# Kernel tuning notes

Measured on AMD Instinct MI355X. Metric: run time of the kernel, lower is better.

## Reference

```python
import jax, jax.numpy as jnp
import numpy as np

NUM_KNOTS = 10
DEGREE = 3
N_POINTS = 8_388_608


def make_knots():
    # Mirrors BSplineBasis.__init__: clamped knot vector on [0, 1]
    inner = np.linspace(0.0, 1.0, NUM_KNOTS - 2 * DEGREE)
    return np.concatenate([np.zeros(DEGREE), inner, np.ones(DEGREE)]).astype(np.float32)


def setup_inputs() -> dict:
    key = jax.random.key(0)
    x = jax.random.normal(key, (N_POINTS,), dtype=jnp.float32)
    knots = jnp.asarray(make_knots())  # [10]
    return {"x": x, "knots": knots}


def bspline_all_bases(x, t, degree):
    """Cox-de Boor recursion evaluating ALL basis functions in one fused pass.

    x: [N] points, t: [K] knots  ->  [N, K-degree-1] basis values.
    Matches scipy BSpline.basis_element per-knot evaluation (zero outside
    support; value 1 at the clamped right endpoint for the last basis).
    """
    K = t.shape[0]
    xe = x[:, None]                       # [N, 1]
    left, right = t[None, :-1], t[None, 1:]
    # degree-0: indicator of half-open interval [t_i, t_{i+1})
    B = ((xe >= left) & (xe < right)).astype(x.dtype)   # [N, K-1]
    # include global right endpoint in the last non-degenerate interval
    B = jnp.where((xe == t[-1]) & (right == t[-1]) & (left < right),
                  jnp.asarray(1.0, x.dtype), B)
    for d in range(1, degree + 1):        # fixed small loop (degree=3)
        tL, tLd = t[: K - d - 1], t[d : K - 1]    # t_i, t_{i+d}
        tR, tRd = t[1 : K - d], t[d + 1 : K]      # t_{i+1}, t_{i+d+1}
        den1 = tLd - tL
        den2 = tRd - tR
        safe1 = jnp.where(den1 > 0, den1, 1.0)
        safe2 = jnp.where(den2 > 0, den2, 1.0)
        w1 = jnp.where(den1[None] > 0, (xe - tL[None]) / safe1[None], 0.0)
        w2 = jnp.where(den2[None] > 0, (tRd[None] - xe) / safe2[None], 0.0)
        B = w1 * B[:, :-1] + w2 * B[:, 1:]        # [N, K-1-d]
    return B                                       # [N, K-degree-1]


def reference(x, knots):
    # forward: min-max normalize to [0,1], then evaluate all B-spline bases
    x_min, x_max = x.min(), x.max()
    x_norm = (x - x_min) / (x_max - x_min + 1e-8)
    return bspline_all_bases(x_norm.ravel(), knots, DEGREE)   # [N, 6]
```

## Files before the change

kernel.cpp:

```cpp
#include <hip/hip_runtime.h>
#include <math.h>

#define NKNOTS 10
#define RED_BLOCKS 1024
#define RED_THREADS 256
#define EVAL_BLOCKS 4096
#define EVAL_THREADS 256


__global__ void reduce_minmax_kernel(const float* __restrict__ x, int n,
                                     float* __restrict__ bmin,
                                     float* __restrict__ bmax) {
    float lmin = INFINITY, lmax = -INFINITY;
    int tid = blockIdx.x * blockDim.x + threadIdx.x;
    int stride = gridDim.x * blockDim.x;
    int n4 = n >> 2;
    const float4* x4 = reinterpret_cast<const float4*>(x);
    for (int i = tid; i < n4; i += stride) {
        float4 v = x4[i];
        lmin = fminf(lmin, fminf(fminf(v.x, v.y), fminf(v.z, v.w)));
        lmax = fmaxf(lmax, fmaxf(fmaxf(v.x, v.y), fmaxf(v.z, v.w)));
    }
    for (int i = (n4 << 2) + tid; i < n; i += stride) {
        float v = x[i];
        lmin = fminf(lmin, v);
        lmax = fmaxf(lmax, v);
    }
#pragma unroll
    for (int off = 32; off > 0; off >>= 1) {
        lmin = fminf(lmin, __shfl_down(lmin, off));
        lmax = fmaxf(lmax, __shfl_down(lmax, off));
    }
    __shared__ float smin[RED_THREADS / 64], smax[RED_THREADS / 64];
    int wave = threadIdx.x >> 6;
    if ((threadIdx.x & 63) == 0) { smin[wave] = lmin; smax[wave] = lmax; }
    __syncthreads();
    if (threadIdx.x == 0) {
        float m = smin[0], M = smax[0];
#pragma unroll
        for (int w = 1; w < RED_THREADS / 64; ++w) {
            m = fminf(m, smin[w]);
            M = fmaxf(M, smax[w]);
        }
        bmin[blockIdx.x] = m;
        bmax[blockIdx.x] = M;
    }
}

__global__ void finalize_kernel(const float* __restrict__ bmin,
                                const float* __restrict__ bmax, int nb,
                                const float* __restrict__ knots,
                                float* __restrict__ params) {
    float lmin = INFINITY, lmax = -INFINITY;
    for (int i = threadIdx.x; i < nb; i += blockDim.x) {
        lmin = fminf(lmin, bmin[i]);
        lmax = fmaxf(lmax, bmax[i]);
    }
#pragma unroll
    for (int off = 32; off > 0; off >>= 1) {
        lmin = fminf(lmin, __shfl_down(lmin, off));
        lmax = fmaxf(lmax, __shfl_down(lmax, off));
    }
    __shared__ float smin[4], smax[4];
    int wave = threadIdx.x >> 6;
    if ((threadIdx.x & 63) == 0) { smin[wave] = lmin; smax[wave] = lmax; }
    __syncthreads();
    if (threadIdx.x == 0) {
        float m = smin[0], M = smax[0];
#pragma unroll
        for (int w = 1; w < 4; ++w) {
            m = fminf(m, smin[w]);
            M = fmaxf(M, smax[w]);
        }
        float denom_f = M - m + 1e-8f;
        double s = 1.0 / (double)denom_f;
        double bb = -(double)m * s;
        double t[NKNOTS];
#pragma unroll
        for (int j = 0; j < NKNOTS; ++j) t[j] = (double)knots[j];

        params[0] = (float)((double)m + t[4] * (double)denom_f);
        params[1] = (float)((double)m + t[5] * (double)denom_f);

        for (int iv = 0; iv < 3; ++iv) {
            double B[9][4];
            for (int j = 0; j < 9; ++j)
                for (int k = 0; k < 4; ++k) B[j][k] = 0.0;
            B[3 + iv][0] = 1.0;
            for (int d = 1; d <= 3; ++d) {
                for (int j = 0; j + d <= 8; ++j) {
                    double den1 = t[j + d] - t[j];
                    double den2 = t[j + d + 1] - t[j + 1];
                    double i1 = (den1 > 0.0) ? 1.0 / den1 : 0.0;
                    double i2 = (den2 > 0.0) ? 1.0 / den2 : 0.0;
                    double a1 = -t[j] * i1, b1 = i1;
                    double a2 = t[j + d + 1] * i2, b2 = -i2;
                    double nb0 = a1 * B[j][0] + a2 * B[j + 1][0];
                    double nb1 = a1 * B[j][1] + b1 * B[j][0] + a2 * B[j + 1][1] + b2 * B[j + 1][0];
                    double nb2 = a1 * B[j][2] + b1 * B[j][1] + a2 * B[j + 1][2] + b2 * B[j + 1][1];
                    double nb3 = a1 * B[j][3] + b1 * B[j][2] + a2 * B[j + 1][3] + b2 * B[j + 1][2];
                    B[j][0] = nb0; B[j][1] = nb1; B[j][2] = nb2; B[j][3] = nb3;
                }
            }
            for (int j = 0; j < 6; ++j) {
                double q0 = B[j][3], q1 = 0.0, q2 = 0.0, q3 = 0.0;
                for (int k = 2; k >= 0; --k) {
                    double r0 = q0 * bb + B[j][k];
                    double r1 = q1 * bb + q0 * s;
                    double r2 = q2 * bb + q1 * s;
                    double r3 = q3 * bb + q2 * s;
                    q0 = r0; q1 = r1; q2 = r2; q3 = r3;
                }
                int base = 4 + (iv * 6 + j) * 4;
                params[base + 0] = (float)q0;
                params[base + 1] = (float)q1;
                params[base + 2] = (float)q2;
                params[base + 3] = (float)q3;
            }
        }
    }
}

__global__ void eval_kernel(const float* __restrict__ x,
                            const float* __restrict__ params,
                            float* __restrict__ out, int n) {
    __shared__ float4 sc4[18];
    if (threadIdx.x < 18)
        sc4[threadIdx.x] = reinterpret_cast<const float4*>(params + 4)[threadIdx.x];
    __syncthreads();
    const float xb1 = params[0], xb2 = params[1];

    int tid = blockIdx.x * blockDim.x + threadIdx.x;
    int stride = gridDim.x * blockDim.x;
    int nquad = n >> 2;
    const float4* x4 = reinterpret_cast<const float4*>(x);
    float4* out4 = reinterpret_cast<float4*>(out);

    for (int p = tid; p < nquad; p += stride) {
        float4 v = x4[p];
        float xs[4] = {v.x, v.y, v.z, v.w};
        float r[4][6];
#pragma unroll
        for (int q = 0; q < 4; ++q) {
            float xv = xs[q];
            int iv = (int)(xv >= xb1) + (int)(xv >= xb2);
            const float4* c4 = sc4 + iv * 6;
#pragma unroll
            for (int j = 0; j < 6; ++j) {
                float4 c = c4[j];
                r[q][j] = ((c.w * xv + c.z) * xv + c.y) * xv + c.x;
            }
        }
        float4* o = out4 + (size_t)p * 6;
        o[0] = make_float4(r[0][0], r[0][1], r[0][2], r[0][3]);
        o[1] = make_float4(r[0][4], r[0][5], r[1][0], r[1][1]);
        o[2] = make_float4(r[1][2], r[1][3], r[1][4], r[1][5]);
        o[3] = make_float4(r[2][0], r[2][1], r[2][2], r[2][3]);
        o[4] = make_float4(r[2][4], r[2][5], r[3][0], r[3][1]);
        o[5] = make_float4(r[3][2], r[3][3], r[3][4], r[3][5]);
    }
    if (tid < (n & 3)) {
        int i = (nquad << 2) + tid;
        float xv = x[i];
        int iv = (int)(xv >= xb1) + (int)(xv >= xb2);
        const float4* c4 = sc4 + iv * 6;
#pragma unroll
        for (int j = 0; j < 6; ++j) {
            float4 c = c4[j];
            out[(size_t)i * 6 + j] = ((c.w * xv + c.z) * xv + c.y) * xv + c.x;
        }
    }
}

extern "C" void kernel_launch(void* const* d_in, const int* in_sizes, int n_in,
                              void* d_out, int out_size, void* d_ws, size_t ws_size,
                              hipStream_t stream) {
    const float* x = (const float*)d_in[0];
    const float* knots = (const float*)d_in[1];
    float* out = (float*)d_out;
    int n = in_sizes[0];

    float* wsf = (float*)d_ws;
    float* params = wsf;
    float* bmin = wsf + 128;
    float* bmax = wsf + 128 + RED_BLOCKS;

    reduce_minmax_kernel<<<RED_BLOCKS, RED_THREADS, 0, stream>>>(x, n, bmin, bmax);
    finalize_kernel<<<1, 256, 0, stream>>>(bmin, bmax, RED_BLOCKS, knots, params);
    eval_kernel<<<EVAL_BLOCKS, EVAL_THREADS, 0, stream>>>(x, params, out, n);
}
```

Before: 259.6 us.

## Stage eval outputs through LDS per wave for fully coalesced float4 stores

The eval kernel now processes two points per lane and writes each lane's three float4 results into a per-wave LDS staging buffer. The wave then stores 192 contiguous float4s, so every lane in a store instruction writes adjacent addresses. Before, each lane wrote six strided float4s. This targets write coalescing on the dominant output stream, at the cost of extra LDS traffic, wave barriers and smaller loads per lane.

```diff
diff --git a/kernel.cpp b/kernel.cpp
--- a/kernel.cpp
+++ b/kernel.cpp
@@ -125,49 +125,76 @@
                             const float* __restrict__ params,
                             float* __restrict__ out, int n) {
     __shared__ float4 sc4[18];
+    __shared__ float4 stage[EVAL_THREADS / 64][192];
     if (threadIdx.x < 18)
         sc4[threadIdx.x] = reinterpret_cast<const float4*>(params + 4)[threadIdx.x];
     __syncthreads();
     const float xb1 = params[0], xb2 = params[1];
 
-    int tid = blockIdx.x * blockDim.x + threadIdx.x;
-    int stride = gridDim.x * blockDim.x;
-    int nquad = n >> 2;
-    const float4* x4 = reinterpret_cast<const float4*>(x);
+    const int lane = threadIdx.x & 63;
+    const int wave = threadIdx.x >> 6;
+    const int gwave = blockIdx.x * (blockDim.x >> 6) + wave;
+    const int nwaves = gridDim.x * (blockDim.x >> 6);
+
+    const int npair = n >> 1;
+    const int nblk = (npair + 63) >> 6;
+    const size_t nf4 = (size_t)npair * 3;
+    const float2* x2 = reinterpret_cast<const float2*>(x);
     float4* out4 = reinterpret_cast<float4*>(out);
-
-    for (int p = tid; p < nquad; p += stride) {
-        float4 v = x4[p];
-        float xs[4] = {v.x, v.y, v.z, v.w};
-        float r[4][6];
-#pragma unroll
-        for (int q = 0; q < 4; ++q) {
-            float xv = xs[q];
-            int iv = (int)(xv >= xb1) + (int)(xv >= xb2);
-            const float4* c4 = sc4 + iv * 6;
-#pragma unroll
-            for (int j = 0; j < 6; ++j) {
-                float4 c = c4[j];
-                r[q][j] = ((c.w * xv + c.z) * xv + c.y) * xv + c.x;
-            }
-        }
-        float4* o = out4 + (size_t)p * 6;
-        o[0] = make_float4(r[0][0], r[0][1], r[0][2], r[0][3]);
-        o[1] = make_float4(r[0][4], r[0][5], r[1][0], r[1][1]);
-        o[2] = make_float4(r[1][2], r[1][3], r[1][4], r[1][5]);
-        o[3] = make_float4(r[2][0], r[2][1], r[2][2], r[2][3]);
-        o[4] = make_float4(r[2][4], r[2][5], r[3][0], r[3][1]);
-        o[5] = make_float4(r[3][2], r[3][3], r[3][4], r[3][5]);
-    }
-    if (tid < (n & 3)) {
-        int i = (nquad << 2) + tid;
-        float xv = x[i];
+    float4* st = stage[wave];
+
+    for (int blk = gwave; blk < nblk; blk += nwaves) {
+        int p = (blk << 6) + lane;
+        float4 s0, s1, s2;
+        if (p < npair) {
+            float2 v = x2[p];
+            float ra[6], rb[6];
+            {
+                float xv = v.x;
+                int iv = (int)(xv >= xb1) + (int)(xv >= xb2);
+                const float4* c4 = sc4 + iv * 6;
+#pragma unroll
+                for (int j = 0; j < 6; ++j) {
+                    float4 c = c4[j];
+                    ra[j] = ((c.w * xv + c.z) * xv + c.y) * xv + c.x;
+                }
+            }
+            {
+                float xv = v.y;
+                int iv = (int)(xv >= xb1) + (int)(xv >= xb2);
+                const float4* c4 = sc4 + iv * 6;
+#pragma unroll
+                for (int j = 0; j < 6; ++j) {
+                    float4 c = c4[j];
+                    rb[j] = ((c.w * xv + c.z) * xv + c.y) * xv + c.x;
+                }
+            }
+            s0 = make_float4(ra[0], ra[1], ra[2], ra[3]);
+            s1 = make_float4(ra[4], ra[5], rb[0], rb[1]);
+            s2 = make_float4(rb[2], rb[3], rb[4], rb[5]);
+        } else {
+            s0 = s1 = s2 = make_float4(0.f, 0.f, 0.f, 0.f);
+        }
+        st[lane * 3 + 0] = s0;
+        st[lane * 3 + 1] = s1;
+        st[lane * 3 + 2] = s2;
+        __builtin_amdgcn_wave_barrier();
+        size_t f0 = (size_t)blk * 192;
+#pragma unroll
+        for (int k = 0; k < 3; ++k) {
+            size_t f = f0 + (size_t)(k << 6) + lane;
+            if (f < nf4) out4[f] = st[(k << 6) + lane];
+        }
+        __builtin_amdgcn_wave_barrier();
+    }
+    if ((n & 1) && blockIdx.x == 0 && threadIdx.x == 0) {
+        float xv = x[n - 1];
         int iv = (int)(xv >= xb1) + (int)(xv >= xb2);
         const float4* c4 = sc4 + iv * 6;
 #pragma unroll
         for (int j = 0; j < 6; ++j) {
             float4 c = c4[j];
-            out[(size_t)i * 6 + j] = ((c.w * xv + c.z) * xv + c.y) * xv + c.x;
+            out[(size_t)(n - 1) * 6 + j] = ((c.w * xv + c.z) * xv + c.y) * xv + c.x;
         }
     }
 }
```

Measured after the change: 235.4 us. -9.3%, faster.
